# Kernel optimization log

Hardware: AMD Instinct MI355X
Metric: run time of the kernel (lower is better)

Reference implementation:

```python
import jax, jax.numpy as jnp
import numpy as np

B, L, D, H, DFF, MODES, ELAYERS = 64, 512, 512, 8, 2048, 32, 2
VOCAB, NUM_APP, KERNEL = 10000, 10000, 25
E = D // H


def setup_inputs() -> dict:
    key = jax.random.key(0)
    ks = jax.random.split(key, 16)
    scale = 1.0 / (D * D)  # FourierBlock weight init scale
    return {
        'x_app': jax.random.randint(ks[0], (B, L), 0, VOCAB),
        'x_time': jax.random.uniform(ks[1], (B, L), dtype=jnp.float32),
        'time_vecs': jax.random.normal(ks[2], (B, L, 24), dtype=jnp.float32),
        'targets': jax.random.randint(ks[3], (B,), 0, NUM_APP),
        'app_emb_w': jax.random.normal(ks[4], (VOCAB, D), dtype=jnp.float32) * 0.02,
        'time_w': jax.random.normal(ks[5], (D,), dtype=jnp.float32) * 0.02,
        'time_b': jnp.zeros((D,), jnp.float32),
        'Wq': jax.random.normal(ks[6], (ELAYERS, D, D), dtype=jnp.float32) * 0.02,
        'bq': jnp.zeros((ELAYERS, D), jnp.float32),
        'Wo': jax.random.normal(ks[7], (ELAYERS, D, D), dtype=jnp.float32) * 0.02,
        'bo': jnp.zeros((ELAYERS, D), jnp.float32),
        'four_wr': jax.random.uniform(ks[8], (ELAYERS, H, E, E, MODES), dtype=jnp.float32) * scale,
        'four_wi': jax.random.uniform(ks[9], (ELAYERS, H, E, E, MODES), dtype=jnp.float32) * scale,
        'conv1_w': jax.random.normal(ks[10], (ELAYERS, DFF, D), dtype=jnp.float32) * 0.02,
        'conv2_w': jax.random.normal(ks[11], (ELAYERS, D, DFF), dtype=jnp.float32) * 0.02,
        'norm_w': jnp.ones((D,), jnp.float32),
        'norm_b': jnp.zeros((D,), jnp.float32),
        'proj_w': jax.random.normal(ks[12], (NUM_APP, D + 24), dtype=jnp.float32) * 0.02,
        'proj_b': jnp.zeros((NUM_APP,), jnp.float32),
    }


def moving_avg(x):
    # edge-replicate pad by (K-1)//2 on each side, then AvgPool1d(K, stride=1)
    pad = (KERNEL - 1) // 2
    xp = jnp.pad(x, ((0, 0), (pad, pad), (0, 0)), mode='edge')  # [B, L+K-1, D]
    cs = jnp.cumsum(xp, axis=1)
    cs = jnp.concatenate([jnp.zeros_like(cs[:, :1]), cs], axis=1)
    return (cs[:, KERNEL:] - cs[:, :-KERNEL]) / KERNEL  # [B, L, D]


def series_decomp(x):
    m = moving_avg(x)
    return x - m, m


def my_layernorm(x, w, b, eps=1e-5):
    mu = jnp.mean(x, axis=-1, keepdims=True)
    var = jnp.mean((x - mu) ** 2, axis=-1, keepdims=True)
    xh = (x - mu) * jax.lax.rsqrt(var + eps) * w + b
    # my_Layernorm: subtract per-sample mean over the sequence dim
    return xh - jnp.mean(xh, axis=1, keepdims=True)


def fourier_block(q, wr, wi):
    # q: [B, L, H, E] -> [B, H, E, L]
    Bq, Lq, Hq, Eq = q.shape
    x = jnp.transpose(q, (0, 2, 3, 1))
    x_ft = jnp.fft.rfft(x, axis=-1)             # [B,H,E,L//2+1] complex64
    xs = x_ft[..., :MODES]                      # low-frequency mode selection
    w = (wr + 1j * wi).astype(xs.dtype)         # [H,E,E,M]
    out_sel = jnp.einsum('bhim,hiom->bhom', xs, w)
    out_ft = jnp.zeros((Bq, Hq, Eq, Lq // 2 + 1), dtype=xs.dtype).at[..., :MODES].set(out_sel)
    return jnp.fft.irfft(out_ft, n=Lq, axis=-1)  # [B,H,E,L]


def encoder_layer(x, Wq, bq, Wo, bo, wr, wi, c1, c2):
    Bx, Lx, Dx = x.shape
    q = (x @ Wq.T + bq).reshape(Bx, Lx, H, E)
    out = fourier_block(q, wr, wi)               # [B,H,E,L]
    # faithful to torch: out.view(B, L, -1) is a raw row-major reinterpret
    out = out.reshape(Bx, Lx, H * E)
    new_x = out @ Wo.T + bo
    x = x + new_x
    x, _ = series_decomp(x)
    y = jax.nn.relu(jnp.einsum('bld,fd->blf', x, c1))   # conv1 (1x1, no bias)
    y = jnp.einsum('blf,df->bld', y, c2)                # conv2 (1x1, no bias)
    res, _ = series_decomp(x + y)
    return res


def reference(x_app, x_time, time_vecs, targets, app_emb_w, time_w, time_b,
              Wq, bq, Wo, bo, four_wr, four_wi, conv1_w, conv2_w,
              norm_w, norm_b, proj_w, proj_b):
    x = app_emb_w[x_app] + x_time[..., None] * time_w + time_b  # [B,L,D]
    for l in range(ELAYERS):
        x = encoder_layer(x, Wq[l], bq[l], Wo[l], bo[l],
                          four_wr[l], four_wi[l], conv1_w[l], conv2_w[l])
    x = my_layernorm(x, norm_w, norm_b)
    last = x[:, -1, :]                                   # [B,D]
    out = jnp.concatenate([last, time_vecs[:, -1, :]], axis=1)  # [B,D+24]
    score = out @ proj_w.T + proj_b                      # [B,NUM_APP]
    return score  # mode='predict' returns score
```

## Files before the change

kernel.cpp:

```cpp
#include <hip/hip_runtime.h>


typedef unsigned short u16;
typedef float f32x4 __attribute__((ext_vector_type(4)));
typedef __bf16 bf16x8 __attribute__((ext_vector_type(8)));

__device__ __forceinline__ u16 f2b(float f) {
  unsigned u = __float_as_uint(f);
  return (u16)((u + 0x7FFFu + ((u >> 16) & 1u)) >> 16);
}
__device__ __forceinline__ float b2f(u16 v) {
  return __uint_as_float((unsigned)v << 16);
}
__device__ __forceinline__ f32x4 b4f(ushort4 v) {
  f32x4 r;
  r.x = b2f(v.x); r.y = b2f(v.y); r.z = b2f(v.z); r.w = b2f(v.w);
  return r;
}

__device__ __forceinline__ void gll16(const void* g, void* l) {
  __builtin_amdgcn_global_load_lds(
      (const __attribute__((address_space(1))) void*)g,
      (__attribute__((address_space(3))) void*)l, 16, 0, 0);
}

template<bool SWAP>
__device__ __forceinline__ f32x4 mfma16(bf16x8 a, bf16x8 b, f32x4 c) {
  if constexpr (SWAP)
    return __builtin_amdgcn_mfma_f32_16x16x32_bf16(b, a, c, 0, 0, 0);
  else
    return __builtin_amdgcn_mfma_f32_16x16x32_bf16(a, b, c, 0, 0, 0);
}

template<bool BIAS, bool RELU, bool RES, bool OUTBF16, bool GUARD, bool TRANS,
         bool SWZ>
__global__ __launch_bounds__(256, 3)
void k_gemm(const u16* __restrict__ A, const u16* __restrict__ B,
            const float* __restrict__ bias, const u16* __restrict__ res,
            float* __restrict__ Cf, u16* __restrict__ Cb,
            int M, int N, int K,
            long zA, long zB, long zC, int nbn, int nbm)
{
  __shared__ __align__(16) u16 sA[2][128 * 32];
  __shared__ __align__(16) u16 sB[2][128 * 32];
  const int tid = threadIdx.x;
  const int wave = tid >> 6, lane = tid & 63;
  int bn, bm;
  if (SWZ) {
    int bid = blockIdx.x;
    int xcd = bid & 7, loc = bid >> 3;
    bn = loc % nbn;
    bm = xcd * (nbm >> 3) + loc / nbn;
  } else {
    bn = blockIdx.x;
    bm = blockIdx.y;
  }
  const int bz = blockIdx.z;
  const int wm = (wave >> 1) * 64, wn = (wave & 1) * 64;

  A += (size_t)bz * zA;
  B += (size_t)bz * zB;

  const int r0 = tid >> 2;
  const int lg = tid & 3;
  const int ps = lg ^ ((r0 >> 1) & 3);
  int gmA0 = bm * 128 + r0, gmA1 = gmA0 + 64;
  int gnB0 = bn * 128 + r0, gnB1 = gnB0 + 64;
  if (GUARD) {
    gmA0 = gmA0 < M ? gmA0 : M - 1;
    gmA1 = gmA1 < M ? gmA1 : M - 1;
    gnB0 = gnB0 < N ? gnB0 : N - 1;
    gnB1 = gnB1 < N ? gnB1 : N - 1;
  }
  const size_t rb = (size_t)K * 2;
  const char* pa0 = (const char*)A + (size_t)gmA0 * rb + lg * 16;
  const char* pa1 = (const char*)A + (size_t)gmA1 * rb + lg * 16;
  const char* pb0 = (const char*)B + (size_t)gnB0 * rb + lg * 16;
  const char* pb1 = (const char*)B + (size_t)gnB1 * rb + lg * 16;
  const int w0 = r0 * 32 + ps * 8;

  f32x4 acc[4][4];
  const f32x4 z = {0.f, 0.f, 0.f, 0.f};
#pragma unroll
  for (int i = 0; i < 4; ++i)
#pragma unroll
    for (int j = 0; j < 4; ++j) acc[i][j] = z;

  const int r = lane & 15, qd = lane >> 4;
  const int pA = (qd ^ ((lane >> 1) & 3)) * 8;
  const int nk = K >> 5;

  uint4 va0, va1, vb0, vb1;
  auto gload = [&](int kt) {
    const size_t ko = (size_t)kt * 64;
    va0 = *(const uint4*)(pa0 + ko);
    va1 = *(const uint4*)(pa1 + ko);
    vb0 = *(const uint4*)(pb0 + ko);
    vb1 = *(const uint4*)(pb1 + ko);
  };

  gload(0);
  int pg = 0;
  for (int kt = 0; kt < nk; ++kt) {
    *(uint4*)&sA[pg][w0]        = va0;
    *(uint4*)&sA[pg][w0 + 2048] = va1;
    *(uint4*)&sB[pg][w0]        = vb0;
    *(uint4*)&sB[pg][w0 + 2048] = vb1;
    if (kt + 1 < nk) gload(kt + 1);
    __syncthreads();
    bf16x8 af[4], bg[4];
#pragma unroll
    for (int mi = 0; mi < 4; ++mi)
      af[mi] = *(const bf16x8*)&sA[pg][(wm + mi * 16 + r) * 32 + pA];
#pragma unroll
    for (int ni = 0; ni < 4; ++ni)
      bg[ni] = *(const bf16x8*)&sB[pg][(wn + ni * 16 + r) * 32 + pA];
#pragma unroll
    for (int mi = 0; mi < 4; ++mi)
#pragma unroll
      for (int ni = 0; ni < 4; ++ni)
        acc[mi][ni] = mfma16<!TRANS>(af[mi], bg[ni], acc[mi][ni]);
    pg ^= 1;
  }

  if (Cf) Cf += (size_t)bz * zC;
  if (Cb) Cb += (size_t)bz * zC;

  if constexpr (!TRANS) {
#pragma unroll
    for (int mi = 0; mi < 4; ++mi) {
      const int gm = bm * 128 + wm + mi * 16 + r;
      if (GUARD && gm >= M) continue;
#pragma unroll
      for (int ni = 0; ni < 4; ++ni) {
        const int gn0 = bn * 128 + wn + ni * 16 + qd * 4;
        if (GUARD && gn0 >= N) continue;
        float v[4];
        ushort4 rv;
        if (RES) rv = *(const ushort4*)&res[(size_t)gm * N + gn0];
#pragma unroll
        for (int e = 0; e < 4; ++e) {
          v[e] = acc[mi][ni][e];
          if (BIAS) v[e] += bias[gn0 + e];
          if (RES)  v[e] += b2f(e == 0 ? rv.x : e == 1 ? rv.y : e == 2 ? rv.z : rv.w);
          if (RELU) v[e] = v[e] > 0.f ? v[e] : 0.f;
        }
        if (OUTBF16) {
          ushort4 o;
          o.x = f2b(v[0]); o.y = f2b(v[1]); o.z = f2b(v[2]); o.w = f2b(v[3]);
          *(ushort4*)&Cb[(size_t)gm * N + gn0] = o;
        } else {
          float4 o = {v[0], v[1], v[2], v[3]};
          *(float4*)&Cf[(size_t)gm * N + gn0] = o;
        }
      }
    }
  } else {
#pragma unroll
    for (int ni = 0; ni < 4; ++ni) {
      const int gn = bn * 128 + wn + ni * 16 + r;
      if (GUARD && gn >= N) continue;
      const float bb = BIAS ? bias[gn] : 0.f;
#pragma unroll
      for (int mi = 0; mi < 4; ++mi) {
        const int gm0 = bm * 128 + wm + mi * 16 + qd * 4;
        if (GUARD && gm0 >= M) continue;
        float v[4];
#pragma unroll
        for (int e = 0; e < 4; ++e) {
          v[e] = acc[mi][ni][e];
          if (BIAS) v[e] += bb;
          if (RELU) v[e] = v[e] > 0.f ? v[e] : 0.f;
        }
        if (OUTBF16) {
          ushort4 o;
          o.x = f2b(v[0]); o.y = f2b(v[1]); o.z = f2b(v[2]); o.w = f2b(v[3]);
          *(ushort4*)&Cb[(size_t)gn * M + gm0] = o;
        } else {
          float4 o = {v[0], v[1], v[2], v[3]};
          *(float4*)&Cf[(size_t)gn * M + gm0] = o;
        }
      }
    }
  }
}

template<bool BIAS, bool RELU, bool RES, bool TRANS>
__global__ __launch_bounds__(512, 2)
void k_gemm3(const u16* __restrict__ A, const u16* __restrict__ B,
             const float* __restrict__ bias, const u16* __restrict__ res,
             u16* __restrict__ C, int M, int N, int K,
             int nbn, int nbm, long zA, long zC)
{
  __shared__ __align__(16) u16 sA[2][2][256 * 32];
  __shared__ __align__(16) u16 sB[2][2][256 * 32];
  const int tid = threadIdx.x;
  const int w8 = tid >> 6, lane = tid & 63;
  const int bid = blockIdx.x;
  const int xcd = bid & 7, loc = bid >> 3;
  const int mpx = (int)(gridDim.x >> 3) / nbn;
  const int mflat = xcd * mpx + loc / nbn;
  const int bn = loc % nbn;
  const int bz = mflat / nbm;
  const int bm = mflat - bz * nbm;
  const int wm = (w8 >> 2) * 128, wn = (w8 & 3) * 64;

  A += (size_t)bz * zA;

  const int r0 = tid >> 2;
  const int lg = (tid & 3) ^ ((r0 >> 1) & 3);
  const u16* pA0 = A + (size_t)(bm * 256 + r0) * K + lg * 8;
  const u16* pA1 = pA0 + (size_t)128 * K;
  const u16* pB0 = B + (size_t)(bn * 256 + r0) * K + lg * 8;
  const u16* pB1 = pB0 + (size_t)128 * K;
  const int la0 = w8 * 512;
  const int la1 = 4096 + w8 * 512;

  const int nk = K >> 6;

  auto stA = [&](int t, int ks) {
    const size_t ko = (size_t)(t << 6) + (size_t)(ks << 5);
    u16* d = &sA[t & 1][ks][0];
    gll16(pA0 + ko, d + la0);
    gll16(pA1 + ko, d + la1);
  };
  auto stB = [&](int t, int ks) {
    const size_t ko = (size_t)(t << 6) + (size_t)(ks << 5);
    u16* d = &sB[t & 1][ks][0];
    gll16(pB0 + ko, d + la0);
    gll16(pB1 + ko, d + la1);
  };

  f32x4 acc[8][4];
  const f32x4 z = {0.f, 0.f, 0.f, 0.f};
#pragma unroll
  for (int i = 0; i < 8; ++i)
#pragma unroll
    for (int j = 0; j < 4; ++j) acc[i][j] = z;

  const int fr = lane & 15, qd = lane >> 4;
  const int pAo = ((qd ^ ((lane >> 1) & 3)) << 3);

  stA(0, 0); stB(0, 0); stA(0, 1); stB(0, 1);
  if (nk > 1) { stA(1, 0); stB(1, 0); }
  asm volatile("s_waitcnt vmcnt(8)" ::: "memory");
  __builtin_amdgcn_s_barrier();

  for (int t = 0; t < nk; ++t) {
    const int c = t & 1;
    bf16x8 af[4], bgk[4];
#pragma unroll
    for (int i = 0; i < 4; ++i)
      af[i] = *(const bf16x8*)&sA[c][0][(wm + i * 16 + fr) * 32 + pAo];
#pragma unroll
    for (int i = 0; i < 4; ++i)
      bgk[i] = *(const bf16x8*)&sB[c][0][(wn + i * 16 + fr) * 32 + pAo];
    if (t + 1 < nk) stA(t + 1, 1);
    asm volatile("s_waitcnt vmcnt(8)" ::: "memory");
    __builtin_amdgcn_s_barrier();
    __builtin_amdgcn_s_setprio(1);
#pragma unroll
    for (int mi = 0; mi < 4; ++mi)
#pragma unroll
      for (int ni = 0; ni < 4; ++ni)
        acc[mi][ni] = mfma16<!TRANS>(af[mi], bgk[ni], acc[mi][ni]);
    __builtin_amdgcn_s_setprio(0);
    __builtin_amdgcn_s_barrier();
#pragma unroll
    for (int i = 0; i < 4; ++i)
      af[i] = *(const bf16x8*)&sA[c][0][(wm + 64 + i * 16 + fr) * 32 + pAo];
    if (t + 1 < nk) stB(t + 1, 1);
    if (t == nk - 1) asm volatile("s_waitcnt vmcnt(0)" ::: "memory");
    else             asm volatile("s_waitcnt vmcnt(8)" ::: "memory");
    __builtin_amdgcn_s_barrier();
    __builtin_amdgcn_s_setprio(1);
#pragma unroll
    for (int mi = 0; mi < 4; ++mi)
#pragma unroll
      for (int ni = 0; ni < 4; ++ni)
        acc[4 + mi][ni] = mfma16<!TRANS>(af[mi], bgk[ni], acc[4 + mi][ni]);
    __builtin_amdgcn_s_setprio(0);
    __builtin_amdgcn_s_barrier();
#pragma unroll
    for (int i = 0; i < 4; ++i)
      af[i] = *(const bf16x8*)&sA[c][1][(wm + i * 16 + fr) * 32 + pAo];
#pragma unroll
    for (int i = 0; i < 4; ++i)
      bgk[i] = *(const bf16x8*)&sB[c][1][(wn + i * 16 + fr) * 32 + pAo];
    if (t + 2 < nk) stA(t + 2, 0);
    asm volatile("s_waitcnt vmcnt(8)" ::: "memory");
    __builtin_amdgcn_s_barrier();
    __builtin_amdgcn_s_setprio(1);
#pragma unroll
    for (int mi = 0; mi < 4; ++mi)
#pragma unroll
      for (int ni = 0; ni < 4; ++ni)
        acc[mi][ni] = mfma16<!TRANS>(af[mi], bgk[ni], acc[mi][ni]);
    __builtin_amdgcn_s_setprio(0);
    __builtin_amdgcn_s_barrier();
#pragma unroll
    for (int i = 0; i < 4; ++i)
      af[i] = *(const bf16x8*)&sA[c][1][(wm + 64 + i * 16 + fr) * 32 + pAo];
    if (t + 2 < nk) stB(t + 2, 0);
    if (t == nk - 2) asm volatile("s_waitcnt vmcnt(4)" ::: "memory");
    else             asm volatile("s_waitcnt vmcnt(8)" ::: "memory");
    __builtin_amdgcn_s_barrier();
    __builtin_amdgcn_s_setprio(1);
#pragma unroll
    for (int mi = 0; mi < 4; ++mi)
#pragma unroll
      for (int ni = 0; ni < 4; ++ni)
        acc[4 + mi][ni] = mfma16<!TRANS>(af[mi], bgk[ni], acc[4 + mi][ni]);
    __builtin_amdgcn_s_setprio(0);
    __builtin_amdgcn_s_barrier();
  }

  C += (size_t)bz * zC;

  if constexpr (!TRANS) {
#pragma unroll
    for (int mi = 0; mi < 8; ++mi) {
      const int gm = bm * 256 + wm + mi * 16 + fr;
#pragma unroll
      for (int ni = 0; ni < 4; ++ni) {
        const int gn0 = bn * 256 + wn + ni * 16 + qd * 4;
        float v[4];
        ushort4 rv;
        if (RES) rv = *(const ushort4*)&res[(size_t)gm * N + gn0];
#pragma unroll
        for (int e = 0; e < 4; ++e) {
          v[e] = acc[mi][ni][e];
          if (BIAS) v[e] += bias[gn0 + e];
          if (RES)  v[e] += b2f(e == 0 ? rv.x : e == 1 ? rv.y : e == 2 ? rv.z : rv.w);
          if (RELU) v[e] = v[e] > 0.f ? v[e] : 0.f;
        }
        ushort4 o;
        o.x = f2b(v[0]); o.y = f2b(v[1]); o.z = f2b(v[2]); o.w = f2b(v[3]);
        *(ushort4*)&C[(size_t)gm * N + gn0] = o;
      }
    }
  } else {
#pragma unroll
    for (int ni = 0; ni < 4; ++ni) {
      const int gn = bn * 256 + wn + ni * 16 + fr;
      const float bb = BIAS ? bias[gn] : 0.f;
#pragma unroll
      for (int mi = 0; mi < 8; ++mi) {
        const int gm0 = bm * 256 + wm + mi * 16 + qd * 4;
        float v[4];
#pragma unroll
        for (int e = 0; e < 4; ++e) {
          v[e] = acc[mi][ni][e];
          if (BIAS) v[e] += bb;
          if (RELU) v[e] = v[e] > 0.f ? v[e] : 0.f;
        }
        ushort4 o;
        o.x = f2b(v[0]); o.y = f2b(v[1]); o.z = f2b(v[2]); o.w = f2b(v[3]);
        *(ushort4*)&C[(size_t)gn * M + gm0] = o;
      }
    }
  }
}

__global__ void k_basis(u16* __restrict__ dftB, u16* __restrict__ Binv)
{
  int id = blockIdx.x * 256 + threadIdx.x;
  if (id >= 32768) return;
  {
    int m = id >> 9, l = id & 511;
    int mm = m & 31;
    float ang = (float)((l * mm) & 511) * (6.283185307179586f / 512.f);
    float s, c;
    __sincosf(ang, &s, &c);
    dftB[id] = f2b(m < 32 ? c : -s);
  }
  {
    int l = id >> 6, m = id & 63;
    int mm = m & 31;
    float ang = (float)((l * mm) & 511) * (6.283185307179586f / 512.f);
    float s, c;
    __sincosf(ang, &s, &c);
    float v;
    if (m < 32) v = (m == 0 ? 1.f : 2.f) * (1.f / 512.f) * c;
    else        v = (mm == 0 ? 0.f : (-2.f / 512.f) * s);
    Binv[id] = f2b(v);
  }
}

__global__ void k_convert(const float* __restrict__ in, u16* __restrict__ out, int n)
{
  int id = blockIdx.x * 256 + threadIdx.x;
  if (id < n) out[id] = f2b(in[id]);
}

__global__ void k_convproj(const float* __restrict__ w, u16* __restrict__ o)
{
  int id = blockIdx.x * 256 + threadIdx.x;
  if (id >= 10000 * 544) return;
  int n = id / 544, k = id % 544;
  o[id] = f2b(k < 536 ? w[(size_t)n * 536 + k] : 0.f);
}

__global__ void k_transp(const float* __restrict__ wr, const float* __restrict__ wi,
                         float* __restrict__ wrT, float* __restrict__ wiT)
{
  __shared__ float tr[64 * 33], ti[64 * 33];
  int blk = blockIdx.x;
  int t = threadIdx.x;
  int lh = blk >> 6, i = blk & 63;
  const size_t src = (size_t)blk * 2048;
#pragma unroll
  for (int p = 0; p < 8; ++p) {
    int id = p * 256 + t;
    int o = id >> 5, m = id & 31;
    tr[o * 33 + m] = wr[src + id];
    ti[o * 33 + m] = wi[src + id];
  }
  __syncthreads();
#pragma unroll
  for (int p = 0; p < 8; ++p) {
    int id = p * 256 + t;
    int m = id >> 6, o = id & 63;
    size_t dst = ((size_t)(lh * 32 + m) * 64 + i) * 64 + o;
    wrT[dst] = tr[o * 33 + m];
    wiT[dst] = ti[o * 33 + m];
  }
}

__global__ void k_embed(const int* __restrict__ xapp, const float* __restrict__ xtime,
                        const float* __restrict__ emb, const float* __restrict__ tw,
                        const float* __restrict__ tb, u16* __restrict__ xb)
{
  int id = blockIdx.x * 256 + threadIdx.x;
  int j = id & 127, bl = id >> 7;
  float4 e = ((const float4*)emb)[(size_t)xapp[bl] * 128 + j];
  float t = xtime[bl];
  float4 w4 = ((const float4*)tw)[j];
  float4 b4 = ((const float4*)tb)[j];
  ushort4 o;
  o.x = f2b(e.x + t * w4.x + b4.x);
  o.y = f2b(e.y + t * w4.y + b4.y);
  o.z = f2b(e.z + t * w4.z + b4.z);
  o.w = f2b(e.w + t * w4.w + b4.w);
  ((ushort4*)xb)[id] = o;
}

__global__ __launch_bounds__(256)
void k_mix(const float* __restrict__ spec, const float* __restrict__ wrT,
           const float* __restrict__ wiT, u16* __restrict__ Ab)
{
  __shared__ float swr[4096], swi[4096];
  __shared__ float sre[4][64], sim[4][64];
  int hm = blockIdx.x;
  int bg = blockIdx.y;
  int h = hm >> 5, m = hm & 31, t = threadIdx.x;
  const float* wrb = wrT + (size_t)hm * 4096;
  const float* wib = wiT + (size_t)hm * 4096;
#pragma unroll
  for (int p = 0; p < 16; ++p) {
    int id = p * 256 + t;
    swr[id] = wrb[id];
    swi[id] = wib[id];
  }
  int o = t & 63, bsub = t >> 6;
  for (int b0 = 0; b0 < 16; b0 += 4) {
    __syncthreads();
    int b = bg * 16 + b0 + bsub;
    const float* spb = spec + (size_t)b * 32768;
    sre[bsub][o] = spb[m * 512 + h * 64 + o];
    sim[bsub][o] = spb[(32 + m) * 512 + h * 64 + o];
    __syncthreads();
    float aR = 0.f, aI = 0.f;
#pragma unroll 8
    for (int i = 0; i < 64; ++i) {
      float xr = sre[bsub][i], xi = sim[bsub][i];
      float wrv = swr[i * 64 + o], wiv = swi[i * 64 + o];
      aR += xr * wrv - xi * wiv;
      aI += xr * wiv + xi * wrv;
    }
    size_t row = (size_t)b * 512 + h * 64 + o;
    Ab[row * 64 + m] = f2b(aR);
    Ab[row * 64 + 32 + m] = f2b(aI);
  }
}

__global__ void k_decomp(const u16* __restrict__ in, u16* __restrict__ outb)
{
  int blk = blockIdx.x;
  int j = blk >> 3;
  int b = (blk & 7) + 8 * (j >> 3);
  int ck = (j & 7) * 2 + (threadIdx.x >> 7);
  int d4 = threadIdx.x & 127;
  const ushort4* xb = (const ushort4*)(in + (size_t)b * 262144) + d4;
  ushort4* ob = (ushort4*)(outb + (size_t)b * 262144) + d4;
  int l0 = ck * 32;
  f32x4 sum = {0.f, 0.f, 0.f, 0.f};
#pragma unroll
  for (int jj = -12; jj <= 12; ++jj) {
    int idx = l0 + jj;
    idx = idx < 0 ? 0 : idx;
    sum += b4f(xb[idx * 128]);
  }
#pragma unroll 4
  for (int l = l0; l < l0 + 32; ++l) {
    f32x4 xv = b4f(xb[l * 128]);
    f32x4 o = xv - sum * (1.f / 25.f);
    ushort4 ov;
    ov.x = f2b(o.x); ov.y = f2b(o.y); ov.z = f2b(o.z); ov.w = f2b(o.w);
    ob[l * 128] = ov;
    int ia = l + 13 > 511 ? 511 : l + 13;
    int ir = l - 12 < 0 ? 0 : l - 12;
    sum += b4f(xb[ia * 128]) - b4f(xb[ir * 128]);
  }
}

__global__ void k_lnstats(const u16* __restrict__ x, float* __restrict__ mu,
                          float* __restrict__ rs)
{
  int row = blockIdx.x;
  const u16* xr = x + (size_t)row * 512;
  int t = threadIdx.x;
  ushort2 p = ((const ushort2*)xr)[t];
  float v0 = b2f(p.x), v1 = b2f(p.y);
  float s = v0 + v1, ss = v0 * v0 + v1 * v1;
#pragma unroll
  for (int off = 32; off; off >>= 1) {
    s += __shfl_down(s, off);
    ss += __shfl_down(ss, off);
  }
  __shared__ float as[4], ass[4];
  if ((t & 63) == 0) { as[t >> 6] = s; ass[t >> 6] = ss; }
  __syncthreads();
  if (t == 0) {
    float S = as[0] + as[1] + as[2] + as[3];
    float SS = ass[0] + ass[1] + ass[2] + ass[3];
    float m = S * (1.f / 512.f);
    float var = SS * (1.f / 512.f) - m * m;
    mu[row] = m;
    rs[row] = rsqrtf(var + 1e-5f);
  }
}

__global__ void k_lastcat1(const u16* __restrict__ x, const float* __restrict__ mu,
                           const float* __restrict__ rs, float* __restrict__ part)
{
  int b = blockIdx.x >> 3, g = blockIdx.x & 7, t = threadIdx.x;
  const u16* xb = x + (size_t)b * 262144;
  const float* mub = mu + b * 512;
  const float* rsb = rs + b * 512;
  float a0 = 0.f, a1 = 0.f;
#pragma unroll 4
  for (int l = g * 64; l < g * 64 + 64; ++l) {
    float m = mub[l], rr = rsb[l];
    ushort2 p = ((const ushort2*)(xb + l * 512))[t];
    a0 += (b2f(p.x) - m) * rr;
    a1 += (b2f(p.y) - m) * rr;
  }
  part[((size_t)b * 8 + g) * 512 + 2 * t]     = a0;
  part[((size_t)b * 8 + g) * 512 + 2 * t + 1] = a1;
}

__global__ void k_lastcat2(const u16* __restrict__ x, const float* __restrict__ mu,
                           const float* __restrict__ rs, const float* __restrict__ part,
                           const float* __restrict__ nw, u16* __restrict__ cat)
{
  int b = blockIdx.x, t = threadIdx.x;
#pragma unroll
  for (int hh = 0; hh < 2; ++hh) {
    int d = t + hh * 256;
    float acc = 0.f;
#pragma unroll
    for (int g = 0; g < 8; ++g)
      acc += part[((size_t)b * 8 + g) * 512 + d];
    float lastv = (b2f(x[(size_t)b * 262144 + 511 * 512 + d]) - mu[b * 512 + 511])
                  * rs[b * 512 + 511];
    cat[b * 544 + d] = f2b(nw[d] * (lastv - acc * (1.f / 512.f)));
  }
}

__global__ void k_timecat(const float* __restrict__ tv, u16* __restrict__ cat)
{
  int id = blockIdx.x * 256 + threadIdx.x;
  if (id >= 2048) return;
  int b = id >> 5, j = id & 31;
  int pos = 512 + j;
  float v = (pos < 536) ? tv[((size_t)b * 512 + 511) * 24 + (pos - 512)] : 0.f;
  cat[b * 544 + pos] = f2b(v);
}

extern "C" void kernel_launch(void* const* d_in, const int* in_sizes, int n_in,
                              void* d_out, int out_size, void* d_ws, size_t ws_size,
                              hipStream_t stream)
{
  (void)in_sizes; (void)n_in; (void)out_size; (void)ws_size;
  const int*   x_app  = (const int*)  d_in[0];
  const float* x_time = (const float*)d_in[1];
  const float* tvec   = (const float*)d_in[2];
  const float* emb    = (const float*)d_in[4];
  const float* time_w = (const float*)d_in[5];
  const float* time_b = (const float*)d_in[6];
  const float* Wq     = (const float*)d_in[7];
  const float* bq     = (const float*)d_in[8];
  const float* Wo     = (const float*)d_in[9];
  const float* bo     = (const float*)d_in[10];
  const float* fwr    = (const float*)d_in[11];
  const float* fwi    = (const float*)d_in[12];
  const float* c1     = (const float*)d_in[13];
  const float* c2     = (const float*)d_in[14];
  const float* norm_w = (const float*)d_in[15];
  const float* proj_w = (const float*)d_in[17];
  const float* proj_b = (const float*)d_in[18];
  float* out = (float*)d_out;

  char* w = (char*)d_ws;
  auto alloc = [&](size_t bytes) -> char* {
    char* p = w;
    w += (bytes + 255) & ~(size_t)255;
    return p;
  };
  u16*   Cb   = (u16*)  alloc(33554432);
  u16*   YqT  = (u16*)  alloc(134217728);
  u16*   T1b  = (u16*)  alloc(33554432);
  float* S1   = (float*)alloc(8388608);
  u16*   Coef = (u16*)  alloc(4194304);
  float* wrT  = (float*)alloc(2 * 1048576 * 4);
  float* wiT  = (float*)alloc(2 * 1048576 * 4);
  u16*   wqb  = (u16*)  alloc(2 * 262144 * 2);
  u16*   wob  = (u16*)  alloc(2 * 262144 * 2);
  u16*   c1b  = (u16*)  alloc(2 * 1048576 * 2);
  u16*   c2b  = (u16*)  alloc(2 * 1048576 * 2);
  u16*   pwb  = (u16*)  alloc(10000 * 544 * 2);
  u16*   dftB = (u16*)  alloc(64 * 512 * 2);
  u16*   Binv = (u16*)  alloc(512 * 64 * 2);
  float* muB  = (float*)alloc(131072);
  float* rsB  = (float*)alloc(131072);
  float* part = (float*)alloc(64 * 8 * 512 * 4);
  u16*   cat  = (u16*)  alloc(64 * 544 * 2);

  k_basis<<<128, 256, 0, stream>>>(dftB, Binv);
  k_transp<<<1024, 256, 0, stream>>>(fwr, fwi, wrT, wiT);
  k_convert<<<2048, 256, 0, stream>>>(Wq, wqb, 524288);
  k_convert<<<2048, 256, 0, stream>>>(Wo, wob, 524288);
  k_convert<<<8192, 256, 0, stream>>>(c1, c1b, 2097152);
  k_convert<<<8192, 256, 0, stream>>>(c2, c2b, 2097152);
  k_convproj<<<21250, 256, 0, stream>>>(proj_w, pwb);
  k_embed<<<16384, 256, 0, stream>>>(x_app, x_time, emb, time_w, time_b, Cb);

  for (int l = 0; l < 2; ++l) {
    const u16* wq_l = wqb + l * 262144;
    const u16* wo_l = wob + l * 262144;
    const u16* c1_l = c1b + l * 1048576;
    const u16* c2_l = c2b + l * 1048576;

    k_gemm3<true, false, false, true>
        <<<256, 512, 0, stream>>>(
        Cb, wq_l, bq + l * 512, nullptr, YqT, 512, 512, 512,
        2, 2, 262144, 262144);
    k_gemm<false, false, false, false, true, true, false>
        <<<dim3(1, 4, 64), 256, 0, stream>>>(
        YqT, dftB, nullptr, nullptr, S1, nullptr, 512, 64, 512,
        262144, 0, 32768, 0, 0);
    k_mix<<<dim3(256, 4), 256, 0, stream>>>(
        S1, wrT + l * 1048576, wiT + l * 1048576, Coef);
    k_gemm<false, false, false, true, false, false, true>
        <<<dim3(1024, 1, 1), 256, 0, stream>>>(
        Coef, Binv, nullptr, nullptr, nullptr, YqT, 32768, 512, 64,
        0, 0, 0, 4, 256);
    k_gemm3<true, false, true, false>
        <<<256, 512, 0, stream>>>(
        YqT, wo_l, bo + l * 512, Cb, T1b, 32768, 512, 512,
        2, 128, 0, 0);
    k_decomp<<<512, 256, 0, stream>>>(T1b, Cb);
    k_gemm3<false, true, false, false>
        <<<1024, 512, 0, stream>>>(
        Cb, c1_l, nullptr, nullptr, YqT, 32768, 2048, 512,
        8, 128, 0, 0);
    k_gemm3<false, false, true, false>
        <<<256, 512, 0, stream>>>(
        YqT, c2_l, nullptr, Cb, T1b, 32768, 512, 2048,
        2, 128, 0, 0);
    k_decomp<<<512, 256, 0, stream>>>(T1b, Cb);
  }

  k_lnstats<<<32768, 256, 0, stream>>>(Cb, muB, rsB);
  k_lastcat1<<<512, 256, 0, stream>>>(Cb, muB, rsB, part);
  k_lastcat2<<<64, 256, 0, stream>>>(Cb, muB, rsB, part, norm_w, cat);
  k_timecat<<<8, 256, 0, stream>>>(tvec, cat);
  k_gemm<true, false, false, false, true, false, false>
      <<<dim3(79, 1, 1), 256, 0, stream>>>(
      cat, pwb, proj_b, nullptr, out, nullptr, 64, 10000, 544,
      0, 0, 0, 0, 0);
}
```

Baseline: 869.2 us.

## Restructure bf16 GEMM to 256x128 tiles with triple-buffered K=32 pipeline

The main bf16 GEMM kernel changes from 256x256 tiles with a double-buffered two-half K=64 schedule to 256x128 tiles. It now uses a three-stage LDS ring over K=32 slices, waits once per iteration and has a simpler prefetch of two slices ahead. The goal is a smaller accumulator and LDS footprint so more blocks fit per CU (launch bounds raised to 4), plus fewer barriers per step. The cost is half the B-tile reuse per block, twice the block count, and only one barrier per step guarding the ring, which may cause extra waiting or reuse hazards.

```diff
diff --git a/kernel.cpp b/kernel.cpp
--- a/kernel.cpp
+++ b/kernel.cpp
@@ -186,14 +186,14 @@
 }
 
 template<bool BIAS, bool RELU, bool RES, bool TRANS>
-__global__ __launch_bounds__(512, 2)
+__global__ __launch_bounds__(512, 4)
 void k_gemm3(const u16* __restrict__ A, const u16* __restrict__ B,
              const float* __restrict__ bias, const u16* __restrict__ res,
              u16* __restrict__ C, int M, int N, int K,
              int nbn, int nbm, long zA, long zC)
 {
-  __shared__ __align__(16) u16 sA[2][2][256 * 32];
-  __shared__ __align__(16) u16 sB[2][2][256 * 32];
+  __shared__ __align__(16) u16 sA[3][256 * 32];
+  __shared__ __align__(16) u16 sB[3][128 * 32];
   const int tid = threadIdx.x;
   const int w8 = tid >> 6, lane = tid & 63;
   const int bid = blockIdx.x;
@@ -203,7 +203,7 @@
   const int bn = loc % nbn;
   const int bz = mflat / nbm;
   const int bm = mflat - bz * nbm;
-  const int wm = (w8 >> 2) * 128, wn = (w8 & 3) * 64;
+  const int wm = (w8 >> 1) * 64, wn = (w8 & 1) * 64;
 
   A += (size_t)bz * zA;
 
@@ -211,119 +211,69 @@
   const int lg = (tid & 3) ^ ((r0 >> 1) & 3);
   const u16* pA0 = A + (size_t)(bm * 256 + r0) * K + lg * 8;
   const u16* pA1 = pA0 + (size_t)128 * K;
-  const u16* pB0 = B + (size_t)(bn * 256 + r0) * K + lg * 8;
-  const u16* pB1 = pB0 + (size_t)128 * K;
+  const u16* pB0 = B + (size_t)(bn * 128 + r0) * K + lg * 8;
   const int la0 = w8 * 512;
   const int la1 = 4096 + w8 * 512;
 
-  const int nk = K >> 6;
-
-  auto stA = [&](int t, int ks) {
-    const size_t ko = (size_t)(t << 6) + (size_t)(ks << 5);
-    u16* d = &sA[t & 1][ks][0];
-    gll16(pA0 + ko, d + la0);
-    gll16(pA1 + ko, d + la1);
+  const int nk = K >> 5;
+
+  auto stage = [&](int t, int sb) {
+    const size_t ko = (size_t)t * 32;
+    gll16(pA0 + ko, &sA[sb][0] + la0);
+    gll16(pA1 + ko, &sA[sb][0] + la1);
+    gll16(pB0 + ko, &sB[sb][0] + la0);
   };
-  auto stB = [&](int t, int ks) {
-    const size_t ko = (size_t)(t << 6) + (size_t)(ks << 5);
-    u16* d = &sB[t & 1][ks][0];
-    gll16(pB0 + ko, d + la0);
-    gll16(pB1 + ko, d + la1);
-  };
-
-  f32x4 acc[8][4];
+
+  f32x4 acc[4][4];
   const f32x4 z = {0.f, 0.f, 0.f, 0.f};
 #pragma unroll
-  for (int i = 0; i < 8; ++i)
+  for (int i = 0; i < 4; ++i)
 #pragma unroll
     for (int j = 0; j < 4; ++j) acc[i][j] = z;
 
   const int fr = lane & 15, qd = lane >> 4;
   const int pAo = ((qd ^ ((lane >> 1) & 3)) << 3);
 
-  stA(0, 0); stB(0, 0); stA(0, 1); stB(0, 1);
-  if (nk > 1) { stA(1, 0); stB(1, 0); }
-  asm volatile("s_waitcnt vmcnt(8)" ::: "memory");
-  __builtin_amdgcn_s_barrier();
-
+  stage(0, 0);
+  stage(1, 1);
+  int cb = 0;
   for (int t = 0; t < nk; ++t) {
-    const int c = t & 1;
-    bf16x8 af[4], bgk[4];
+    if (t + 1 < nk) asm volatile("s_waitcnt vmcnt(3)" ::: "memory");
+    else            asm volatile("s_waitcnt vmcnt(0)" ::: "memory");
+    __builtin_amdgcn_s_barrier();
+    asm volatile("" ::: "memory");
+    const u16* bufA = &sA[cb][0];
+    const u16* bufB = &sB[cb][0];
+    bf16x8 af[4], bg[4];
 #pragma unroll
     for (int i = 0; i < 4; ++i)
-      af[i] = *(const bf16x8*)&sA[c][0][(wm + i * 16 + fr) * 32 + pAo];
+      af[i] = *(const bf16x8*)&bufA[(wm + i * 16 + fr) * 32 + pAo];
 #pragma unroll
     for (int i = 0; i < 4; ++i)
-      bgk[i] = *(const bf16x8*)&sB[c][0][(wn + i * 16 + fr) * 32 + pAo];
-    if (t + 1 < nk) stA(t + 1, 1);
-    asm volatile("s_waitcnt vmcnt(8)" ::: "memory");
-    __builtin_amdgcn_s_barrier();
+      bg[i] = *(const bf16x8*)&bufB[(wn + i * 16 + fr) * 32 + pAo];
+    if (t + 2 < nk) {
+      int sb = cb + 2; if (sb >= 3) sb -= 3;
+      stage(t + 2, sb);
+    }
     __builtin_amdgcn_s_setprio(1);
 #pragma unroll
     for (int mi = 0; mi < 4; ++mi)
 #pragma unroll
       for (int ni = 0; ni < 4; ++ni)
-        acc[mi][ni] = mfma16<!TRANS>(af[mi], bgk[ni], acc[mi][ni]);
+        acc[mi][ni] = mfma16<!TRANS>(af[mi], bg[ni], acc[mi][ni]);
     __builtin_amdgcn_s_setprio(0);
-    __builtin_amdgcn_s_barrier();
-#pragma unroll
-    for (int i = 0; i < 4; ++i)
-      af[i] = *(const bf16x8*)&sA[c][0][(wm + 64 + i * 16 + fr) * 32 + pAo];
-    if (t + 1 < nk) stB(t + 1, 1);
-    if (t == nk - 1) asm volatile("s_waitcnt vmcnt(0)" ::: "memory");
-    else             asm volatile("s_waitcnt vmcnt(8)" ::: "memory");
-    __builtin_amdgcn_s_barrier();
-    __builtin_amdgcn_s_setprio(1);
-#pragma unroll
-    for (int mi = 0; mi < 4; ++mi)
-#pragma unroll
-      for (int ni = 0; ni < 4; ++ni)
-        acc[4 + mi][ni] = mfma16<!TRANS>(af[mi], bgk[ni], acc[4 + mi][ni]);
-    __builtin_amdgcn_s_setprio(0);
-    __builtin_amdgcn_s_barrier();
-#pragma unroll
-    for (int i = 0; i < 4; ++i)
-      af[i] = *(const bf16x8*)&sA[c][1][(wm + i * 16 + fr) * 32 + pAo];
-#pragma unroll
-    for (int i = 0; i < 4; ++i)
-      bgk[i] = *(const bf16x8*)&sB[c][1][(wn + i * 16 + fr) * 32 + pAo];
-    if (t + 2 < nk) stA(t + 2, 0);
-    asm volatile("s_waitcnt vmcnt(8)" ::: "memory");
-    __builtin_amdgcn_s_barrier();
-    __builtin_amdgcn_s_setprio(1);
-#pragma unroll
-    for (int mi = 0; mi < 4; ++mi)
-#pragma unroll
-      for (int ni = 0; ni < 4; ++ni)
-        acc[mi][ni] = mfma16<!TRANS>(af[mi], bgk[ni], acc[mi][ni]);
-    __builtin_amdgcn_s_setprio(0);
-    __builtin_amdgcn_s_barrier();
-#pragma unroll
-    for (int i = 0; i < 4; ++i)
-      af[i] = *(const bf16x8*)&sA[c][1][(wm + 64 + i * 16 + fr) * 32 + pAo];
-    if (t + 2 < nk) stB(t + 2, 0);
-    if (t == nk - 2) asm volatile("s_waitcnt vmcnt(4)" ::: "memory");
-    else             asm volatile("s_waitcnt vmcnt(8)" ::: "memory");
-    __builtin_amdgcn_s_barrier();
-    __builtin_amdgcn_s_setprio(1);
-#pragma unroll
-    for (int mi = 0; mi < 4; ++mi)
-#pragma unroll
-      for (int ni = 0; ni < 4; ++ni)
-        acc[4 + mi][ni] = mfma16<!TRANS>(af[mi], bgk[ni], acc[4 + mi][ni]);
-    __builtin_amdgcn_s_setprio(0);
-    __builtin_amdgcn_s_barrier();
+    cb = (cb == 2) ? 0 : cb + 1;
   }
 
   C += (size_t)bz * zC;
 
   if constexpr (!TRANS) {
 #pragma unroll
-    for (int mi = 0; mi < 8; ++mi) {
+    for (int mi = 0; mi < 4; ++mi) {
       const int gm = bm * 256 + wm + mi * 16 + fr;
 #pragma unroll
       for (int ni = 0; ni < 4; ++ni) {
-        const int gn0 = bn * 256 + wn + ni * 16 + qd * 4;
+        const int gn0 = bn * 128 + wn + ni * 16 + qd * 4;
         float v[4];
         ushort4 rv;
         if (RES) rv = *(const ushort4*)&res[(size_t)gm * N + gn0];
@@ -342,10 +292,10 @@
   } else {
 #pragma unroll
     for (int ni = 0; ni < 4; ++ni) {
-      const int gn = bn * 256 + wn + ni * 16 + fr;
+      const int gn = bn * 128 + wn + ni * 16 + fr;
       const float bb = BIAS ? bias[gn] : 0.f;
 #pragma unroll
-      for (int mi = 0; mi < 8; ++mi) {
+      for (int mi = 0; mi < 4; ++mi) {
         const int gm0 = bm * 256 + wm + mi * 16 + qd * 4;
         float v[4];
 #pragma unroll
@@ -653,9 +603,9 @@
     const u16* c2_l = c2b + l * 1048576;
 
     k_gemm3<true, false, false, true>
-        <<<256, 512, 0, stream>>>(
+        <<<512, 512, 0, stream>>>(
         Cb, wq_l, bq + l * 512, nullptr, YqT, 512, 512, 512,
-        2, 2, 262144, 262144);
+        4, 2, 262144, 262144);
     k_gemm<false, false, false, false, true, true, false>
         <<<dim3(1, 4, 64), 256, 0, stream>>>(
         YqT, dftB, nullptr, nullptr, S1, nullptr, 512, 64, 512,
@@ -667,18 +617,18 @@
         Coef, Binv, nullptr, nullptr, nullptr, YqT, 32768, 512, 64,
         0, 0, 0, 4, 256);
     k_gemm3<true, false, true, false>
-        <<<256, 512, 0, stream>>>(
+        <<<512, 512, 0, stream>>>(
         YqT, wo_l, bo + l * 512, Cb, T1b, 32768, 512, 512,
-        2, 128, 0, 0);
+        4, 128, 0, 0);
     k_decomp<<<512, 256, 0, stream>>>(T1b, Cb);
     k_gemm3<false, true, false, false>
-        <<<1024, 512, 0, stream>>>(
+        <<<2048, 512, 0, stream>>>(
         Cb, c1_l, nullptr, nullptr, YqT, 32768, 2048, 512,
-        8, 128, 0, 0);
+        16, 128, 0, 0);
     k_gemm3<false, false, true, false>
-        <<<256, 512, 0, stream>>>(
+        <<<512, 512, 0, stream>>>(
         YqT, c2_l, nullptr, Cb, T1b, 32768, 512, 2048,
-        2, 128, 0, 0);
+        4, 128, 0, 0);
     k_decomp<<<512, 256, 0, stream>>>(T1b, Cb);
   }
 
```

After: 872.6 us. No clear change (+0.4%).
